# Kernel tuning notes

Hardware: AMD Instinct MI355X
Metric: run time of the kernel (lower is better)

The kernel has to match this reference:

```python
import jax, jax.numpy as jnp
import numpy as np

N = 100000
D = 128          # atom_input_dim
OUT = 256        # output_dim
HOPS = 3
E = 640000
IN_DIM = D * (HOPS + 1)  # 512


def setup_inputs() -> dict:
    key = jax.random.key(0)
    ks = jax.random.split(key, 16)
    s = 0.02
    inp = {
        "x": jax.random.normal(ks[0], (N, D), dtype=jnp.float32),
        "target": jax.random.randint(ks[1], (E,), 0, HOPS * N, dtype=jnp.int64),
        "src": jax.random.randint(ks[2], (E,), 0, HOPS * N, dtype=jnp.int64),
        "W_in": jax.random.normal(ks[3], (IN_DIM, OUT), dtype=jnp.float32) * s,
        "b_in": jnp.zeros((OUT,), dtype=jnp.float32),
        "W1_0": jax.random.normal(ks[4], (OUT, OUT), dtype=jnp.float32) * s,
        "b1_0": jnp.zeros((OUT,), dtype=jnp.float32),
        "W2_0": jax.random.normal(ks[5], (OUT, OUT), dtype=jnp.float32) * s,
        "b2_0": jnp.zeros((OUT,), dtype=jnp.float32),
        "W1_1": jax.random.normal(ks[6], (OUT, OUT), dtype=jnp.float32) * s,
        "b1_1": jnp.zeros((OUT,), dtype=jnp.float32),
        "W2_1": jax.random.normal(ks[7], (OUT, OUT), dtype=jnp.float32) * s,
        "b2_1": jnp.zeros((OUT,), dtype=jnp.float32),
        "W_skip": jax.random.normal(ks[8], (IN_DIM, OUT), dtype=jnp.float32) * s,
        "b_skip": jnp.zeros((OUT,), dtype=jnp.float32),
    }
    return inp


def reference(x, target, src, W_in, b_in, W1_0, b1_0, W2_0, b2_0,
              W1_1, b1_1, W2_1, b2_1, W_skip, b_skip):
    n = x.shape[0]
    # multi-hop message passing: tile node features HOPS times, gather by src,
    # scatter-add into target over the tiled index space [0, HOPS*n)
    expanded = jnp.tile(x, (HOPS, 1))                       # [HOPS*n, D]
    agg = jnp.zeros_like(expanded).at[target].add(expanded[src])
    # split per-hop chunks and concat with original features -> [n, (HOPS+1)*D]
    feats = jnp.concatenate([x] + [agg[h * n:(h + 1) * n] for h in range(HOPS)], axis=-1)
    h = jax.nn.silu(feats @ W_in + b_in)                    # [n, OUT]
    global_skip = feats @ W_skip + b_skip                   # input_dim != output_dim
    for W1, b1, W2, b2 in ((W1_0, b1_0, W2_0, b2_0), (W1_1, b1_1, W2_1, b2_1)):
        h = (jax.nn.silu(h @ W1 + b1)) @ W2 + b2 + h        # residual MLP block (dropout=0)
    return h + global_skip
```

## Files before the change

### kernel.cpp

```cpp
#include <hip/hip_runtime.h>
#include <math.h>

#define NN 100000
#define DD 128
#define OUT_DIM 256
#define HOPS 3
#define EDGES 640000
#define TGT (HOPS*NN)

typedef short bf16x8 __attribute__((ext_vector_type(8)));
typedef float f32x4 __attribute__((ext_vector_type(4)));

__device__ __forceinline__ unsigned short f2bf(float f) {
    unsigned u = __float_as_uint(f);
    unsigned r = u + 0x7FFFu + ((u >> 16) & 1u);
    return (unsigned short)(r >> 16);
}
__device__ __forceinline__ float bf2f(unsigned short s) {
    return __uint_as_float(((unsigned)s) << 16);
}
__device__ __forceinline__ float silu(float v) { return v / (1.0f + expf(-v)); }

__device__ __forceinline__ void gload16(const unsigned short* g, unsigned short* l) {
    __builtin_amdgcn_global_load_lds(
        (const __attribute__((address_space(1))) void*)g,
        (__attribute__((address_space(3))) void*)l, 16, 0, 0);
}

__global__ __launch_bounds__(256) void k_hist(const int* __restrict__ tgt,
                                              int* __restrict__ cnt) {
    int e = blockIdx.x * 256 + threadIdx.x;
    atomicAdd(&cnt[tgt[e]], 1);
}

__global__ __launch_bounds__(512) void k_scanb(const int* __restrict__ cnt,
                                               int* __restrict__ off,
                                               int* __restrict__ part, int n) {
    __shared__ int s[512];
    int tid = threadIdx.x;
    int g = blockIdx.x * 512 + tid;
    int v = (g < n) ? cnt[g] : 0;
    s[tid] = v;
    __syncthreads();
    for (int d = 1; d < 512; d <<= 1) {
        int a = (tid >= d) ? s[tid - d] : 0;
        __syncthreads();
        s[tid] += a;
        __syncthreads();
    }
    if (g < n) off[g] = s[tid] - v;
    if (tid == 511) part[blockIdx.x] = s[511];
}

__global__ __launch_bounds__(1024) void k_scanp(int* __restrict__ part, int n) {
    __shared__ int s[1024];
    int t = threadIdx.x;
    s[t] = (t < n) ? part[t] : 0;
    __syncthreads();
    for (int d = 1; d < 1024; d <<= 1) {
        int a = (t >= d) ? s[t - d] : 0;
        __syncthreads();
        s[t] += a;
        __syncthreads();
    }
    if (t < n) part[t] = s[t];
}

__global__ __launch_bounds__(512) void k_addoff(int* __restrict__ off,
                                                const int* __restrict__ part,
                                                int* __restrict__ cursor, int n) {
    int g = blockIdx.x * 512 + threadIdx.x;
    if (g >= n) return;
    int add = (blockIdx.x > 0) ? part[blockIdx.x - 1] : 0;
    int o = off[g] + add;
    off[g] = o;
    cursor[g] = o;
}

__global__ __launch_bounds__(256) void k_fill(const int* __restrict__ tgt,
                                              const int* __restrict__ src,
                                              int* __restrict__ cursor,
                                              int* __restrict__ esrc) {
    int e = blockIdx.x * 256 + threadIdx.x;
    int t = tgt[e];
    int p = atomicAdd(&cursor[t], 1);
    esrc[p] = src[e] % NN;
}

__global__ __launch_bounds__(256) void k_aggfeats(const float* __restrict__ x,
                                                  const int* __restrict__ off,
                                                  const int* __restrict__ cur,
                                                  const int* __restrict__ esrc,
                                                  unsigned* __restrict__ feats) {
    int lane = threadIdx.x & 63;
    int r = blockIdx.x * 4 + (threadIdx.x >> 6);
    const float2* x2 = (const float2*)x;
    if (r < NN) {
        float2 v = x2[(size_t)r * 64 + lane];
        feats[(size_t)r * 256 + lane] =
            (unsigned)f2bf(v.x) | ((unsigned)f2bf(v.y) << 16);
    } else {
        int t = r - NN;
        int hop = t / NN;
        int tn = t - hop * NN;
        int b = off[t], e = cur[t];
        float ax = 0.f, ay = 0.f;
        for (int i = b; i < e; ++i) {
            int sn = esrc[i];
            float2 v = x2[(size_t)sn * 64 + lane];
            ax += v.x; ay += v.y;
        }
        feats[(size_t)tn * 256 + 64 + hop * 64 + lane] =
            (unsigned)f2bf(ax) | ((unsigned)f2bf(ay) << 16);
    }
}

__global__ __launch_bounds__(256) void k_wprep(
    const float* __restrict__ Win, const float* __restrict__ Wskip,
    const float* __restrict__ W10, const float* __restrict__ W20,
    const float* __restrict__ W11, const float* __restrict__ W21,
    unsigned short* __restrict__ Wt1, unsigned short* __restrict__ Wt25) {
    int idx = blockIdx.x * 256 + threadIdx.x;
    if (idx < 262144) {
        int c = idx >> 9, k = idx & 511;
        float v = (c < 256) ? Win[k * 256 + c] : Wskip[k * 256 + (c - 256)];
        Wt1[idx] = f2bf(v);
    } else {
        int j = idx - 262144;
        int m = j >> 16, rr = j & 65535;
        int c = rr >> 8, k = rr & 255;
        const float* Wm = (m == 0) ? W10 : (m == 1) ? W20 : (m == 2) ? W11 : W21;
        Wt25[(size_t)m * 65536 + c * 256 + k] = f2bf(Wm[k * 256 + c]);
    }
}

template <int K, int EPI>
__global__ __launch_bounds__(256) void k_gemm_t(
    const unsigned short* __restrict__ A, const unsigned short* __restrict__ Wt,
    const float* __restrict__ bias0, const float* __restrict__ bias1,
    const unsigned short* __restrict__ res1, const float* __restrict__ res2,
    unsigned short* __restrict__ Cb, float* __restrict__ Cf) {
    __shared__ unsigned short As[128 * 64];
    __shared__ unsigned short Bs[128 * 64];

    const int tid = threadIdx.x;
    const int lane = tid & 63;
    const int w = tid >> 6;
    const int row0 = blockIdx.x * 128;
    const int col0 = blockIdx.y * 128;

    const int wr = (w >> 1) * 64;
    const int wc = (w & 1) * 64;
    const int lr = lane & 15;
    const int lk8 = (lane >> 4) * 8;

    f32x4 acc[4][4];
    #pragma unroll
    for (int m = 0; m < 4; ++m)
        #pragma unroll
        for (int n = 0; n < 4; ++n) acc[m][n] = (f32x4){0.f, 0.f, 0.f, 0.f};

    for (int k0 = 0; k0 < K; k0 += 64) {
        #pragma unroll
        for (int i = 0; i < 4; ++i) {
            int chunk = i * 4 + w;
            int slot = chunk * 64 + lane;
            int r = slot >> 3;
            int kq = (slot & 7) * 8;
            gload16(A + (size_t)(row0 + r) * K + k0 + kq, As + chunk * 512);
            gload16(Wt + (size_t)(col0 + r) * K + k0 + kq, Bs + chunk * 512);
        }
        asm volatile("s_waitcnt vmcnt(0)" ::: "memory");
        __syncthreads();

        #pragma unroll
        for (int ks2 = 0; ks2 < 2; ++ks2) {
            bf16x8 af[4], bfr[4];
            #pragma unroll
            for (int m = 0; m < 4; ++m)
                af[m] = *(const bf16x8*)&As[(wr + m * 16 + lr) * 64 + ks2 * 32 + lk8];
            #pragma unroll
            for (int n = 0; n < 4; ++n)
                bfr[n] = *(const bf16x8*)&Bs[(wc + n * 16 + lr) * 64 + ks2 * 32 + lk8];
            #pragma unroll
            for (int m = 0; m < 4; ++m)
                #pragma unroll
                for (int n = 0; n < 4; ++n)
                    acc[m][n] = __builtin_amdgcn_mfma_f32_16x16x32_bf16(
                        af[m], bfr[n], acc[m][n], 0, 0, 0);
        }
        __syncthreads();
    }

    const int rq = (lane >> 4) * 4;
    #pragma unroll
    for (int m = 0; m < 4; ++m) {
        #pragma unroll
        for (int n = 0; n < 4; ++n) {
            int cg = col0 + wc + n * 16 + lr;
            float bb = (EPI == 3 && cg >= OUT_DIM) ? bias1[cg - OUT_DIM] : bias0[cg < OUT_DIM ? cg : 0];
            #pragma unroll
            for (int j = 0; j < 4; ++j) {
                int r = row0 + wr + m * 16 + rq + j;
                if (r >= NN) continue;
                float v = acc[m][n][j] + bb;
                if (EPI == 3) {
                    if (cg < OUT_DIM)
                        Cb[(size_t)r * OUT_DIM + cg] = f2bf(silu(v));
                    else
                        Cf[(size_t)r * OUT_DIM + (cg - OUT_DIM)] = v;
                } else if (EPI == 0) {
                    Cb[(size_t)r * OUT_DIM + cg] = f2bf(silu(v));
                } else if (EPI == 1) {
                    size_t o = (size_t)r * OUT_DIM + cg;
                    Cb[o] = f2bf(v + bf2f(res1[o]));
                } else {
                    size_t o = (size_t)r * OUT_DIM + cg;
                    Cf[o] = v + bf2f(res1[o]) + res2[o];
                }
            }
        }
    }
}

extern "C" void kernel_launch(void* const* d_in, const int* in_sizes, int n_in,
                              void* d_out, int out_size, void* d_ws, size_t ws_size,
                              hipStream_t stream) {
    const float* x      = (const float*)d_in[0];
    const int*   target = (const int*)d_in[1];
    const int*   src    = (const int*)d_in[2];
    const float* W_in   = (const float*)d_in[3];
    const float* b_in   = (const float*)d_in[4];
    const float* W1_0   = (const float*)d_in[5];
    const float* b1_0   = (const float*)d_in[6];
    const float* W2_0   = (const float*)d_in[7];
    const float* b2_0   = (const float*)d_in[8];
    const float* W1_1   = (const float*)d_in[9];
    const float* b1_1   = (const float*)d_in[10];
    const float* W2_1   = (const float*)d_in[11];
    const float* b2_1   = (const float*)d_in[12];
    const float* W_skip = (const float*)d_in[13];
    const float* b_skip = (const float*)d_in[14];
    float* out = (float*)d_out;

    char* p = (char*)d_ws;
    unsigned short* feats = (unsigned short*)p; p += (size_t)NN * 512 * 2;
    unsigned short* h0    = (unsigned short*)p; p += (size_t)NN * 256 * 2;
    unsigned short* h1    = (unsigned short*)p; p += (size_t)NN * 256 * 2;
    unsigned short* tb    = (unsigned short*)p; p += (size_t)NN * 256 * 2;
    unsigned short* Wt1   = (unsigned short*)p; p += 512 * 512 * 2;
    unsigned short* Wt25  = (unsigned short*)p; p += 4 * 256 * 256 * 2;
    int* cnt    = (int*)p; p += (size_t)TGT * 4;
    int* off    = (int*)p; p += (size_t)TGT * 4;
    int* cursor = (int*)p; p += (size_t)TGT * 4;
    int* esrc   = (int*)p; p += (size_t)EDGES * 4;
    int* part   = (int*)p; p += 4096;

    const int SCAN_BLOCKS = (TGT + 511) / 512;

    hipMemsetAsync(cnt, 0, (size_t)TGT * 4, stream);
    k_hist<<<EDGES / 256, 256, 0, stream>>>(target, cnt);
    k_scanb<<<SCAN_BLOCKS, 512, 0, stream>>>(cnt, off, part, TGT);
    k_scanp<<<1, 1024, 0, stream>>>(part, SCAN_BLOCKS);
    k_addoff<<<SCAN_BLOCKS, 512, 0, stream>>>(off, part, cursor, TGT);
    k_fill<<<EDGES / 256, 256, 0, stream>>>(target, src, cursor, esrc);

    k_aggfeats<<<NN, 256, 0, stream>>>(x, off, cursor, esrc, (unsigned*)feats);

    k_wprep<<<2048, 256, 0, stream>>>(W_in, W_skip, W1_0, W2_0, W1_1, W2_1,
                                      Wt1, Wt25);

    const int GM = (NN + 127) / 128;

    k_gemm_t<512, 3><<<dim3(GM, 4), 256, 0, stream>>>(
        feats, Wt1, b_in, b_skip, nullptr, nullptr, h0, out);

    k_gemm_t<256, 0><<<dim3(GM, 2), 256, 0, stream>>>(
        h0, Wt25 + 0 * 65536, b1_0, nullptr, nullptr, nullptr, tb, nullptr);
    k_gemm_t<256, 1><<<dim3(GM, 2), 256, 0, stream>>>(
        tb, Wt25 + 1 * 65536, b2_0, nullptr, h0, nullptr, h1, nullptr);

    k_gemm_t<256, 0><<<dim3(GM, 2), 256, 0, stream>>>(
        h1, Wt25 + 2 * 65536, b1_1, nullptr, nullptr, nullptr, tb, nullptr);
    k_gemm_t<256, 2><<<dim3(GM, 2), 256, 0, stream>>>(
        tb, Wt25 + 3 * 65536, b2_1, nullptr, h1, out, nullptr, out);
}
```

Before: 787.9 us.

## Swizzle bf16 activation/weight layouts and double-buffer GEMM LDS tiles

```diff
diff --git a/kernel.cpp b/kernel.cpp
--- a/kernel.cpp
+++ b/kernel.cpp
@@ -20,6 +20,10 @@
     return __uint_as_float(((unsigned)s) << 16);
 }
 __device__ __forceinline__ float silu(float v) { return v / (1.0f + expf(-v)); }
+
+__device__ __forceinline__ int swz(int c, int r) {
+    return (c & ~63) | ((c & 63) ^ ((r & 7) << 3));
+}
 
 __device__ __forceinline__ void gload16(const unsigned short* g, unsigned short* l) {
     __builtin_amdgcn_global_load_lds(
@@ -97,7 +101,9 @@
     const float2* x2 = (const float2*)x;
     if (r < NN) {
         float2 v = x2[(size_t)r * 64 + lane];
-        feats[(size_t)r * 256 + lane] =
+        int p = lane;
+        int ps = (p & ~31) | ((p & 31) ^ ((r & 7) << 2));
+        feats[(size_t)r * 256 + ps] =
             (unsigned)f2bf(v.x) | ((unsigned)f2bf(v.y) << 16);
     } else {
         int t = r - NN;
@@ -110,7 +116,9 @@
             float2 v = x2[(size_t)sn * 64 + lane];
             ax += v.x; ay += v.y;
         }
-        feats[(size_t)tn * 256 + 64 + hop * 64 + lane] =
+        int p = 64 + hop * 64 + lane;
+        int ps = (p & ~31) | ((p & 31) ^ ((tn & 7) << 2));
+        feats[(size_t)tn * 256 + ps] =
             (unsigned)f2bf(ax) | ((unsigned)f2bf(ay) << 16);
     }
 }
@@ -123,14 +131,16 @@
     int idx = blockIdx.x * 256 + threadIdx.x;
     if (idx < 262144) {
         int c = idx >> 9, k = idx & 511;
-        float v = (c < 256) ? Win[k * 256 + c] : Wskip[k * 256 + (c - 256)];
+        int kl = swz(k, c);
+        float v = (c < 256) ? Win[kl * 256 + c] : Wskip[kl * 256 + (c - 256)];
         Wt1[idx] = f2bf(v);
     } else {
         int j = idx - 262144;
         int m = j >> 16, rr = j & 65535;
         int c = rr >> 8, k = rr & 255;
+        int kl = swz(k, c);
         const float* Wm = (m == 0) ? W10 : (m == 1) ? W20 : (m == 2) ? W11 : W21;
-        Wt25[(size_t)m * 65536 + c * 256 + k] = f2bf(Wm[k * 256 + c]);
+        Wt25[(size_t)m * 65536 + c * 256 + k] = f2bf(Wm[kl * 256 + c]);
     }
 }
 
@@ -140,8 +150,8 @@
     const float* __restrict__ bias0, const float* __restrict__ bias1,
     const unsigned short* __restrict__ res1, const float* __restrict__ res2,
     unsigned short* __restrict__ Cb, float* __restrict__ Cf) {
-    __shared__ unsigned short As[128 * 64];
-    __shared__ unsigned short Bs[128 * 64];
+    __shared__ unsigned short As[2][128 * 64];
+    __shared__ unsigned short Bs[2][128 * 64];
 
     const int tid = threadIdx.x;
     const int lane = tid & 63;
@@ -160,28 +170,43 @@
         #pragma unroll
         for (int n = 0; n < 4; ++n) acc[m][n] = (f32x4){0.f, 0.f, 0.f, 0.f};
 
-    for (int k0 = 0; k0 < K; k0 += 64) {
+    const int NK = K / 64;
+
+    auto STAGE = [&](int buf, int k0) {
         #pragma unroll
         for (int i = 0; i < 4; ++i) {
             int chunk = i * 4 + w;
             int slot = chunk * 64 + lane;
             int r = slot >> 3;
             int kq = (slot & 7) * 8;
-            gload16(A + (size_t)(row0 + r) * K + k0 + kq, As + chunk * 512);
-            gload16(Wt + (size_t)(col0 + r) * K + k0 + kq, Bs + chunk * 512);
+            gload16(A + (size_t)(row0 + r) * K + k0 + kq, &As[buf][chunk * 512]);
+            gload16(Wt + (size_t)(col0 + r) * K + k0 + kq, &Bs[buf][chunk * 512]);
         }
-        asm volatile("s_waitcnt vmcnt(0)" ::: "memory");
-        __syncthreads();
+    };
+
+    STAGE(0, 0);
+    asm volatile("s_waitcnt vmcnt(0)" ::: "memory");
+    __syncthreads();
+
+    for (int ks = 0; ks < NK; ++ks) {
+        int cur = ks & 1;
+        if (ks + 1 < NK) STAGE(cur ^ 1, (ks + 1) * 64);
 
         #pragma unroll
         for (int ks2 = 0; ks2 < 2; ++ks2) {
             bf16x8 af[4], bfr[4];
             #pragma unroll
-            for (int m = 0; m < 4; ++m)
-                af[m] = *(const bf16x8*)&As[(wr + m * 16 + lr) * 64 + ks2 * 32 + lk8];
+            for (int m = 0; m < 4; ++m) {
+                int row = wr + m * 16 + lr;
+                int eo = (ks2 * 32 + lk8) ^ ((row & 7) << 3);
+                af[m] = *(const bf16x8*)&As[cur][row * 64 + eo];
+            }
             #pragma unroll
-            for (int n = 0; n < 4; ++n)
-                bfr[n] = *(const bf16x8*)&Bs[(wc + n * 16 + lr) * 64 + ks2 * 32 + lk8];
+            for (int n = 0; n < 4; ++n) {
+                int row = wc + n * 16 + lr;
+                int eo = (ks2 * 32 + lk8) ^ ((row & 7) << 3);
+                bfr[n] = *(const bf16x8*)&Bs[cur][row * 64 + eo];
+            }
             #pragma unroll
             for (int m = 0; m < 4; ++m)
                 #pragma unroll
@@ -189,6 +214,7 @@
                     acc[m][n] = __builtin_amdgcn_mfma_f32_16x16x32_bf16(
                         af[m], bfr[n], acc[m][n], 0, 0, 0);
         }
+        asm volatile("s_waitcnt vmcnt(0)" ::: "memory");
         __syncthreads();
     }
 
@@ -198,7 +224,9 @@
         #pragma unroll
         for (int n = 0; n < 4; ++n) {
             int cg = col0 + wc + n * 16 + lr;
-            float bb = (EPI == 3 && cg >= OUT_DIM) ? bias1[cg - OUT_DIM] : bias0[cg < OUT_DIM ? cg : 0];
+            float bb = (EPI == 3)
+                           ? (cg < OUT_DIM ? bias0[cg] : bias1[cg - OUT_DIM])
+                           : bias0[cg];
             #pragma unroll
             for (int j = 0; j < 4; ++j) {
                 int r = row0 + wr + m * 16 + rq + j;
@@ -206,17 +234,18 @@
                 float v = acc[m][n][j] + bb;
                 if (EPI == 3) {
                     if (cg < OUT_DIM)
-                        Cb[(size_t)r * OUT_DIM + cg] = f2bf(silu(v));
+                        Cb[(size_t)r * OUT_DIM + swz(cg, r)] = f2bf(silu(v));
                     else
                         Cf[(size_t)r * OUT_DIM + (cg - OUT_DIM)] = v;
                 } else if (EPI == 0) {
-                    Cb[(size_t)r * OUT_DIM + cg] = f2bf(silu(v));
+                    Cb[(size_t)r * OUT_DIM + swz(cg, r)] = f2bf(silu(v));
                 } else if (EPI == 1) {
-                    size_t o = (size_t)r * OUT_DIM + cg;
+                    size_t o = (size_t)r * OUT_DIM + swz(cg, r);
                     Cb[o] = f2bf(v + bf2f(res1[o]));
                 } else {
-                    size_t o = (size_t)r * OUT_DIM + cg;
-                    Cf[o] = v + bf2f(res1[o]) + res2[o];
+                    size_t os = (size_t)r * OUT_DIM + swz(cg, r);
+                    size_t ol = (size_t)r * OUT_DIM + cg;
+                    Cf[ol] = v + bf2f(res1[os]) + res2[ol];
                 }
             }
         }
```

Result: slower. 823.3 us (+4.5%).
